# Optimization experiments

Measured on AMD Instinct MI355X. Metric: run time of the kernel, lower is better.

Reference implementation:

```python
import jax, jax.numpy as jnp
import numpy as np

A, B, S, E, H = 8, 64, 128, 512, 512


def _xavier(key, shape):
    fan_in, fan_out = shape[-2], shape[-1]
    limit = float(np.sqrt(6.0 / (fan_in + fan_out)))
    return jax.random.uniform(key, shape, jnp.float32, -limit, limit)


def setup_inputs() -> dict:
    key = jax.random.key(0)
    ks = jax.random.split(key, 8)
    inp = {
        "x": jax.random.normal(ks[0], (A, B, S, E), jnp.float32),
        "input2r": _xavier(ks[1], (A, E, H)),
        "input2z": _xavier(ks[2], (A, E, H)),
        "input2n": _xavier(ks[3], (A, E, H)),
        "hidden2r": _xavier(ks[4], (A, H, H)),
        "hidden2z": _xavier(ks[5], (A, H, H)),
        "hidden2n": _xavier(ks[6], (A, H, H)),
        "input2r_bias": jnp.zeros((A, H), jnp.float32),
        "input2z_bias": jnp.zeros((A, H), jnp.float32),
        "input2n_bias": jnp.zeros((A, H), jnp.float32),
        "hidden2r_bias": jnp.zeros((A, H), jnp.float32),
        "hidden2z_bias": jnp.zeros((A, H), jnp.float32),
        "hidden2n_bias": jnp.zeros((A, H), jnp.float32),
    }
    return inp


def _gru(x, input2r, input2z, input2n, input2r_bias, input2z_bias, input2n_bias,
         hidden2r, hidden2z, hidden2n, hidden2r_bias, hidden2z_bias, hidden2n_bias):
    # Precompute the input projections for all timesteps at once (same math,
    # hoisted out of the sequential loop): [A,B,S,H] -> scan over S.
    xr = jnp.einsum('abse,aeh->absh', x, input2r) + input2r_bias[:, None, None, :]
    xz = jnp.einsum('abse,aeh->absh', x, input2z) + input2z_bias[:, None, None, :]
    xn = jnp.einsum('abse,aeh->absh', x, input2n) + input2n_bias[:, None, None, :]
    # scan carries h: [A,B,H]; inputs have leading S axis.
    xr_t = jnp.moveaxis(xr, 2, 0)  # [S,A,B,H]
    xz_t = jnp.moveaxis(xz, 2, 0)
    xn_t = jnp.moveaxis(xn, 2, 0)

    hrb = hidden2r_bias[:, None, :]
    hzb = hidden2z_bias[:, None, :]
    hnb = hidden2n_bias[:, None, :]

    def step(h, inputs):
        xr_i, xz_i, xn_i = inputs
        r = jax.nn.sigmoid(xr_i + jnp.einsum('abh,ahk->abk', h, hidden2r) + hrb)
        z = jax.nn.sigmoid(xz_i + jnp.einsum('abh,ahk->abk', h, hidden2z) + hzb)
        n = jnp.tanh(xn_i + r * (jnp.einsum('abh,ahk->abk', h, hidden2n) + hnb))
        h_new = (1.0 - z) * n + z * h
        return h_new, h_new

    h0 = jnp.zeros((x.shape[0], x.shape[1], hidden2r.shape[-1]), x.dtype)
    h_last, outs = jax.lax.scan(step, h0, (xr_t, xz_t, xn_t))
    outputs = jnp.moveaxis(outs, 0, 2)  # [A,B,S,H]
    return outputs, h_last


def reference(x, input2r, input2z, input2n, input2r_bias, input2z_bias, input2n_bias,
              hidden2r, hidden2z, hidden2n, hidden2r_bias, hidden2z_bias, hidden2n_bias):
    return _gru(x, input2r, input2z, input2n, input2r_bias, input2z_bias, input2n_bias,
                hidden2r, hidden2z, hidden2n, hidden2r_bias, hidden2z_bias, hidden2n_bias)
```

## Files before the change

### kernel.cpp

```cpp
#include <hip/hip_runtime.h>

#define A_ 8
#define B_ 64
#define S_ 128
#define E_ 512
#define H_ 512

typedef float f32x4 __attribute__((ext_vector_type(4)));
typedef short s16x8 __attribute__((ext_vector_type(8)));

__device__ __forceinline__ float sigm(float v)   { return 1.f / (1.f + __expf(-v)); }
__device__ __forceinline__ float tanh_f(float v) { return 2.f / (1.f + __expf(-2.f * v)) - 1.f; }

__device__ __forceinline__ unsigned short f2bf(float f) {
  unsigned u = __builtin_bit_cast(unsigned, f);
  u += 0x7fffu + ((u >> 16) & 1u);
  return (unsigned short)(u >> 16);
}
__device__ __forceinline__ float bf2f(unsigned short b) {
  return __builtin_bit_cast(float, ((unsigned)b) << 16);
}

union U2 { unsigned long long u[2]; s16x8 v; };
union PK { uint4 u; unsigned short h[8]; };
union PH { s16x8 v; unsigned short h[8]; };

__global__ __launch_bounds__(256, 2) void gru_proj(
    const float* __restrict__ x,
    const float* __restrict__ wri, const float* __restrict__ wzi, const float* __restrict__ wni,
    const float* __restrict__ bri, const float* __restrict__ bzi, const float* __restrict__ bni,
    const float* __restrict__ brh, const float* __restrict__ bzh,
    unsigned short* __restrict__ xprz, float* __restrict__ xn_arr)
{
  const int b    = blockIdx.x;
  const int gate = blockIdx.y >> 2;
  const int n0   = (blockIdx.y & 3) * 128;
  const int a    = blockIdx.z;
  const int tid  = threadIdx.x;
  const int lane = tid & 63;
  const int wid  = tid >> 6;
  const int l15  = lane & 15;
  const int l4   = lane >> 4;

  const float* W  = gate == 0 ? wri : gate == 1 ? wzi : wni;
  const float* Wp = W + (size_t)a * E_ * H_;
  const float* xp = x + (size_t)(a * B_ + b) * S_ * E_;

  __shared__ short Af[4096];
  __shared__ short Bf[4096];

  f32x4 acc[2][8];
#pragma unroll
  for (int i = 0; i < 2; ++i)
#pragma unroll
    for (int j = 0; j < 8; ++j) acc[i][j] = (f32x4){0.f, 0.f, 0.f, 0.f};

  const int am  = tid >> 1;
  const int ah  = tid & 1;
  const int bnl = tid & 127;
  const int bo2 = (tid >> 7) * 2;

  for (int kt = 0; kt < E_; kt += 32) {
    const float* ap = xp + (size_t)am * E_ + kt + ah * 16;
    float4 a0 = *(const float4*)(ap);
    float4 a1 = *(const float4*)(ap + 4);
    float4 a2 = *(const float4*)(ap + 8);
    float4 a3 = *(const float4*)(ap + 12);
    PH pa0, pa1;
    pa0.h[0]=f2bf(a0.x); pa0.h[1]=f2bf(a0.y); pa0.h[2]=f2bf(a0.z); pa0.h[3]=f2bf(a0.w);
    pa0.h[4]=f2bf(a1.x); pa0.h[5]=f2bf(a1.y); pa0.h[6]=f2bf(a1.z); pa0.h[7]=f2bf(a1.w);
    pa1.h[0]=f2bf(a2.x); pa1.h[1]=f2bf(a2.y); pa1.h[2]=f2bf(a2.z); pa1.h[3]=f2bf(a2.w);
    pa1.h[4]=f2bf(a3.x); pa1.h[5]=f2bf(a3.y); pa1.h[6]=f2bf(a3.z); pa1.h[7]=f2bf(a3.w);
    int au = (am >> 4) * 64 + (ah * 2) * 16 + (am & 15);
    ((s16x8*)Af)[au]      = pa0.v;
    ((s16x8*)Af)[au + 16] = pa1.v;
#pragma unroll
    for (int oo = 0; oo < 2; ++oo) {
      int o = bo2 + oo;
      const float* wp2 = Wp + (size_t)(kt + o * 8) * H_ + n0 + bnl;
      PH pb;
#pragma unroll
      for (int j = 0; j < 8; ++j) pb.h[j] = f2bf(wp2[(size_t)j * H_]);
      ((s16x8*)Bf)[(bnl >> 4) * 64 + o * 16 + (bnl & 15)] = pb.v;
    }
    __syncthreads();
    s16x8 av0 = ((s16x8*)Af)[(wid * 2 + 0) * 64 + lane];
    s16x8 av1 = ((s16x8*)Af)[(wid * 2 + 1) * 64 + lane];
#pragma unroll
    for (int ns = 0; ns < 8; ++ns) {
      s16x8 bv = ((s16x8*)Bf)[ns * 64 + lane];
      acc[0][ns] = __builtin_amdgcn_mfma_f32_16x16x32_bf16(av0, bv, acc[0][ns], 0, 0, 0);
      acc[1][ns] = __builtin_amdgcn_mfma_f32_16x16x32_bf16(av1, bv, acc[1][ns], 0, 0, 0);
    }
    __syncthreads();
  }

#pragma unroll
  for (int ns = 0; ns < 8; ++ns) {
    int col = n0 + ns * 16 + l15;
    float bv;
    if (gate == 0)      bv = bri[a * H_ + col] + brh[a * H_ + col];
    else if (gate == 1) bv = bzi[a * H_ + col] + bzh[a * H_ + col];
    else                bv = bni[a * H_ + col];
#pragma unroll
    for (int ms = 0; ms < 2; ++ms) {
#pragma unroll
      for (int i = 0; i < 4; ++i) {
        int srow = wid * 32 + ms * 16 + l4 * 4 + i;
        size_t base = ((size_t)(a * S_ + srow) * B_ + b) * H_ + col;
        float v = acc[ms][ns][i] + bv;
        if (gate == 2) xn_arr[base] = v;
        else           xprz[base * 2 + gate] = f2bf(v);
      }
    }
  }
}

__global__ __launch_bounds__(256, 1) void gru_scan(
    const unsigned* __restrict__ xprz, const float* __restrict__ xn_arr,
    const float* __restrict__ wrh, const float* __restrict__ wzh, const float* __restrict__ wnh,
    const float* __restrict__ bnh,
    float* __restrict__ out, float* __restrict__ hlast,
    unsigned short* __restrict__ hbuf0, unsigned short* __restrict__ hbuf1,
    int* __restrict__ flags)
{
  __shared__ uint4 wflat[6144];

  const int wg    = blockIdx.x;
  const int G     = wg & 15;
  const int a     = G >> 1;
  const int hf    = G & 1;
  const int slice = wg >> 4;
  const int tid   = threadIdx.x;
  const int lane  = tid & 63;
  const int w     = tid >> 6;
  const int l15   = lane & 15;
  const int l4    = lane >> 4;
  const int mt    = w & 1;
  const int nt    = w >> 1;

  for (int idx = tid; idx < 6144; idx += 256) {
    int gate = idx >> 11;
    int rem  = idx & 2047;
    int kk   = rem >> 7;
    int rem2 = rem & 127;
    int nt_  = rem2 >> 6;
    int l    = rem2 & 63;
    int col   = slice * 32 + nt_ * 16 + (l & 15);
    int kbase = kk * 32 + (l >> 4) * 8;
    const float* W = gate == 0 ? wrh : gate == 1 ? wzh : wnh;
    const float* wp = W + ((size_t)(a * H_ + kbase)) * H_ + col;
    PK pk;
#pragma unroll
    for (int j = 0; j < 8; ++j) pk.h[j] = f2bf(wp[(size_t)j * H_]);
    wflat[idx] = pk.u;
  }
  __syncthreads();

  const int nc    = slice * 32 + nt * 16 + l15;
  const float vbnh = bnh[a * H_ + nc];
  const int halfb = (a * 2 + hf) * 16384;
  const int hbase = halfb + l4 * 256 + (mt * 16 + l15) * 8;
  int* flagsG = flags + G * (16 * 32);

  float hold[4] = {0.f, 0.f, 0.f, 0.f};
  float xr_[4], xz_[4], xn_[4];

#pragma unroll
  for (int i = 0; i < 4; ++i) {
    int b = hf * 32 + mt * 16 + l4 * 4 + i;
    size_t xo = ((size_t)(a * S_ + 0) * B_ + b) * H_ + nc;
    unsigned prz = xprz[xo];
    xr_[i] = bf2f((unsigned short)(prz & 0xffff));
    xz_[i] = bf2f((unsigned short)(prz >> 16));
    xn_[i] = xn_arr[xo];
  }

  const f32x4 zero4 = {0.f, 0.f, 0.f, 0.f};

  for (int s = 0; s < S_; ++s) {
    const unsigned short* hprev = (s & 1) ? hbuf0 : hbuf1;
    unsigned short*       hcur  = (s & 1) ? hbuf1 : hbuf0;

    U2 hh[16];
#pragma unroll
    for (int kk = 0; kk < 16; ++kk) {
      unsigned long long* p = (unsigned long long*)(hprev + hbase + kk * 1024);
      hh[kk].u[0] = __hip_atomic_load(p,     __ATOMIC_RELAXED, __HIP_MEMORY_SCOPE_AGENT);
      hh[kk].u[1] = __hip_atomic_load(p + 1, __ATOMIC_RELAXED, __HIP_MEMORY_SCOPE_AGENT);
    }
    f32x4 aR = zero4, aZ = zero4, aHN = zero4;
#pragma unroll
    for (int kk = 0; kk < 16; ++kk) {
      s16x8 bR = __builtin_bit_cast(s16x8, wflat[(kk)*128        + nt * 64 + lane]);
      s16x8 bZ = __builtin_bit_cast(s16x8, wflat[2048 + kk * 128 + nt * 64 + lane]);
      s16x8 bN = __builtin_bit_cast(s16x8, wflat[4096 + kk * 128 + nt * 64 + lane]);
      aR  = __builtin_amdgcn_mfma_f32_16x16x32_bf16(hh[kk].v, bR, aR, 0, 0, 0);
      aZ  = __builtin_amdgcn_mfma_f32_16x16x32_bf16(hh[kk].v, bZ, aZ, 0, 0, 0);
      aHN = __builtin_amdgcn_mfma_f32_16x16x32_bf16(hh[kk].v, bN, aHN, 0, 0, 0);
    }

    float hn4[4];
#pragma unroll
    for (int i = 0; i < 4; ++i) {
      float rg = sigm(xr_[i] + aR[i]);
      float zg = sigm(xz_[i] + aZ[i]);
      float ng = tanh_f(xn_[i] + rg * (aHN[i] + vbnh));
      hn4[i] = (1.f - zg) * ng + zg * hold[i];
      hold[i] = hn4[i];
    }

#pragma unroll
    for (int i = 0; i < 4; ++i) {
      int r = mt * 16 + l4 * 4 + i;
      unsigned short nb = f2bf(hn4[i]);
      unsigned other = __shfl_xor((unsigned)nb, 1);
      if ((lane & 1) == 0) {
        unsigned val = (unsigned)nb | (other << 16);
        __hip_atomic_store((unsigned*)(hcur + halfb + (nc >> 3) * 256 + r * 8 + (nc & 6)),
                           val, __ATOMIC_RELAXED, __HIP_MEMORY_SCOPE_AGENT);
      }
    }
    __syncthreads();
    asm volatile("" ::: "memory");
    if (tid == 0)
      __hip_atomic_store(flagsG + slice * 32, s + 1,
                         __ATOMIC_RELAXED, __HIP_MEMORY_SCOPE_AGENT);

#pragma unroll
    for (int i = 0; i < 4; ++i) {
      int b = hf * 32 + mt * 16 + l4 * 4 + i;
      out[((size_t)(a * B_ + b) * S_ + s) * H_ + nc] = hn4[i];
    }
    if (s == S_ - 1) {
#pragma unroll
      for (int i = 0; i < 4; ++i) {
        int b = hf * 32 + mt * 16 + l4 * 4 + i;
        hlast[(size_t)(a * B_ + b) * H_ + nc] = hn4[i];
      }
    } else {
#pragma unroll
      for (int i = 0; i < 4; ++i) {
        int b = hf * 32 + mt * 16 + l4 * 4 + i;
        size_t xo = ((size_t)(a * S_ + (s + 1)) * B_ + b) * H_ + nc;
        unsigned prz = xprz[xo];
        xr_[i] = bf2f((unsigned short)(prz & 0xffff));
        xz_[i] = bf2f((unsigned short)(prz >> 16));
        xn_[i] = xn_arr[xo];
      }
      const int target = s + 1;
      for (;;) {
        int v = __hip_atomic_load(flagsG + (lane & 15) * 32,
                                  __ATOMIC_RELAXED, __HIP_MEMORY_SCOPE_AGENT);
        if (__all(v >= target)) break;
      }
      asm volatile("" ::: "memory");
    }
  }
}

__global__ __launch_bounds__(256, 1) void gru_persist(
    const float* __restrict__ x,
    const float* __restrict__ wri, const float* __restrict__ wzi, const float* __restrict__ wni,
    const float* __restrict__ wrh, const float* __restrict__ wzh, const float* __restrict__ wnh,
    const float* __restrict__ bri, const float* __restrict__ bzi, const float* __restrict__ bni,
    const float* __restrict__ brh, const float* __restrict__ bzh, const float* __restrict__ bnh,
    float* __restrict__ out, float* __restrict__ hlast,
    unsigned short* __restrict__ hbuf0, unsigned short* __restrict__ hbuf1,
    int* __restrict__ flags)
{
  __shared__ uint4 wflat[6144];
  const int wg = blockIdx.x, a = wg >> 5, slice = wg & 31, n0 = slice << 4;
  const int tid = threadIdx.x, lane = tid & 63, wid = tid >> 6;
  const int l15 = lane & 15, l4 = lane >> 4, b0w = wid << 4;

  for (int idx = tid; idx < 6144; idx += 256) {
    int set = idx / 3072, rem = idx - set * 3072, gate = rem >> 10;
    int rem2 = rem & 1023, kk = rem2 >> 6, l = rem2 & 63;
    int c = l & 15, kbase = kk * 32 + (l >> 4) * 8;
    const float* W = (set == 0) ? (gate == 0 ? wri : gate == 1 ? wzi : wni)
                                : (gate == 0 ? wrh : gate == 1 ? wzh : wnh);
    const float* wp = W + ((size_t)(a * 512 + kbase)) * 512 + n0 + c;
    PK pk;
#pragma unroll
    for (int j = 0; j < 8; ++j) pk.h[j] = f2bf(wp[(size_t)j * 512]);
    wflat[idx] = pk.u;
  }
  __syncthreads();

  const int nc = n0 + l15;
  const float vbri = bri[a*512+nc], vbzi = bzi[a*512+nc], vbni = bni[a*512+nc];
  const float vbrh = brh[a*512+nc], vbzh = bzh[a*512+nc], vbnh = bnh[a*512+nc];
  const float* xrow = x + (size_t)(a * 64 + b0w + l15) * 65536 + l4 * 8;
  const int hbase = ((a * 64 + l4) * 64 + b0w + l15) * 8;
  int* flagsA = flags + a * 64;
  const f32x4 zero4 = {0.f, 0.f, 0.f, 0.f};
  f32x4 aR, aZ, aXN, aHN;

  auto xpart = [&](int sv) {
    const float* xp = xrow + (size_t)sv * 512;
    aR = zero4; aZ = zero4; aXN = zero4;
#pragma unroll
    for (int kk = 0; kk < 16; ++kk) {
      float4 x0 = *reinterpret_cast<const float4*>(xp + kk * 32);
      float4 x1 = *reinterpret_cast<const float4*>(xp + kk * 32 + 4);
      PH af;
      af.h[0]=f2bf(x0.x); af.h[1]=f2bf(x0.y); af.h[2]=f2bf(x0.z); af.h[3]=f2bf(x0.w);
      af.h[4]=f2bf(x1.x); af.h[5]=f2bf(x1.y); af.h[6]=f2bf(x1.z); af.h[7]=f2bf(x1.w);
      s16x8 bR = __builtin_bit_cast(s16x8, wflat[(kk)*64+lane]);
      s16x8 bZ = __builtin_bit_cast(s16x8, wflat[(16+kk)*64+lane]);
      s16x8 bN = __builtin_bit_cast(s16x8, wflat[(32+kk)*64+lane]);
      aR  = __builtin_amdgcn_mfma_f32_16x16x32_bf16(af.v, bR, aR, 0,0,0);
      aZ  = __builtin_amdgcn_mfma_f32_16x16x32_bf16(af.v, bZ, aZ, 0,0,0);
      aXN = __builtin_amdgcn_mfma_f32_16x16x32_bf16(af.v, bN, aXN, 0,0,0);
    }
  };

  xpart(0);
  for (int s = 0; s < S_; ++s) {
    const unsigned short* hprev = (s & 1) ? hbuf0 : hbuf1;
    unsigned short*       hcur  = (s & 1) ? hbuf1 : hbuf0;
    aHN = zero4;
#pragma unroll
    for (int kk = 0; kk < 16; ++kk) {
      unsigned long long* p = (unsigned long long*)(hprev + hbase + kk * 2048);
      U2 uu;
      uu.u[0] = __hip_atomic_load(p,   __ATOMIC_RELAXED, __HIP_MEMORY_SCOPE_AGENT);
      uu.u[1] = __hip_atomic_load(p+1, __ATOMIC_RELAXED, __HIP_MEMORY_SCOPE_AGENT);
      s16x8 bR = __builtin_bit_cast(s16x8, wflat[(48+kk)*64+lane]);
      s16x8 bZ = __builtin_bit_cast(s16x8, wflat[(64+kk)*64+lane]);
      s16x8 bN = __builtin_bit_cast(s16x8, wflat[(80+kk)*64+lane]);
      aR  = __builtin_amdgcn_mfma_f32_16x16x32_bf16(uu.v, bR, aR, 0,0,0);
      aZ  = __builtin_amdgcn_mfma_f32_16x16x32_bf16(uu.v, bZ, aZ, 0,0,0);
      aHN = __builtin_amdgcn_mfma_f32_16x16x32_bf16(uu.v, bN, aHN, 0,0,0);
    }
#pragma unroll
    for (int i = 0; i < 4; ++i) {
      int r = b0w + l4 * 4 + i;
      unsigned* hop = (unsigned*)(hprev + ((a*64 + (nc>>3))*64 + r)*8 + (nc&6));
      unsigned pair = __hip_atomic_load(hop, __ATOMIC_RELAXED, __HIP_MEMORY_SCOPE_AGENT);
      float hold = bf2f((nc & 1) ? (unsigned short)(pair >> 16) : (unsigned short)(pair & 0xffff));
      float rg = sigm(aR[i] + vbri + vbrh);
      float zg = sigm(aZ[i] + vbzi + vbzh);
      float ng = tanh_f(aXN[i] + vbni + rg * (aHN[i] + vbnh));
      float hnew = (1.f - zg) * ng + zg * hold;
      out[((size_t)(a*64 + r)*128 + s)*512 + nc] = hnew;
      if (s == S_ - 1) hlast[(size_t)(a*64 + r)*512 + nc] = hnew;
      unsigned short nb = f2bf(hnew);
      unsigned other = __shfl_xor((unsigned)nb, 1);
      if ((lane & 1) == 0) {
        unsigned val = (unsigned)nb | (other << 16);
        __hip_atomic_store((unsigned*)(hcur + ((a*64 + (nc>>3))*64 + r)*8 + (nc&6)),
                           val, __ATOMIC_RELAXED, __HIP_MEMORY_SCOPE_AGENT);
      }
    }
    __syncthreads();
    if (tid == 0)
      __hip_atomic_store(flagsA + slice, s + 1, __ATOMIC_RELEASE, __HIP_MEMORY_SCOPE_AGENT);
    if (s < S_ - 1) {
      xpart(s + 1);
      const int target = s + 1;
      for (;;) {
        int v = __hip_atomic_load(flagsA + (lane & 31), __ATOMIC_ACQUIRE, __HIP_MEMORY_SCOPE_AGENT);
        if (__all(v >= target)) break;
        __builtin_amdgcn_s_sleep(1);
      }
    }
  }
}

extern "C" void kernel_launch(void* const* d_in, const int* in_sizes, int n_in,
                              void* d_out, int out_size, void* d_ws, size_t ws_size,
                              hipStream_t stream)
{
  const float* x   = (const float*)d_in[0];
  const float* wri = (const float*)d_in[1];
  const float* wzi = (const float*)d_in[2];
  const float* wni = (const float*)d_in[3];
  const float* wrh = (const float*)d_in[4];
  const float* wzh = (const float*)d_in[5];
  const float* wnh = (const float*)d_in[6];
  const float* bri = (const float*)d_in[7];
  const float* bzi = (const float*)d_in[8];
  const float* bni = (const float*)d_in[9];
  const float* brh = (const float*)d_in[10];
  const float* bzh = (const float*)d_in[11];
  const float* bnh = (const float*)d_in[12];

  float* out   = (float*)d_out;
  float* hlast = out + (size_t)A_ * B_ * S_ * H_;

  const size_t XPRZ  = (size_t)A_ * S_ * B_ * H_;
  const size_t HBUF  = (size_t)A_ * 64 * 64 * 8;
  const size_t FLAGS_B = (size_t)16 * 16 * 32 * sizeof(int);
  const size_t need_new = XPRZ * 4 * 2 + HBUF * 2 * 2 + FLAGS_B;
  const size_t need_old = HBUF * 2 * 2 + 2048;

  if (ws_size >= need_new) {
    unsigned* xprz = (unsigned*)d_ws;
    float* xn_arr  = (float*)((char*)d_ws + XPRZ * 4);
    unsigned short* hbuf0 = (unsigned short*)((char*)d_ws + XPRZ * 8);
    unsigned short* hbuf1 = hbuf0 + HBUF;
    int* flags = (int*)(hbuf1 + HBUF);
    hipMemsetAsync(hbuf0, 0, HBUF * 2 * 2 + FLAGS_B, stream);
    gru_proj<<<dim3(64, 12, 8), 256, 0, stream>>>(x, wri, wzi, wni,
                                                  bri, bzi, bni, brh, bzh,
                                                  (unsigned short*)xprz, xn_arr);
    gru_scan<<<256, 256, 0, stream>>>(xprz, xn_arr, wrh, wzh, wnh, bnh,
                                      out, hlast, hbuf0, hbuf1, flags);
  } else if (ws_size >= need_old) {
    unsigned short* hbuf0 = (unsigned short*)d_ws;
    unsigned short* hbuf1 = hbuf0 + HBUF;
    int* flags = (int*)(hbuf1 + HBUF);
    hipMemsetAsync(d_ws, 0, need_old, stream);
    gru_persist<<<256, 256, 0, stream>>>(x, wri, wzi, wni, wrh, wzh, wnh,
                                         bri, bzi, bni, brh, bzh, bnh,
                                         out, hlast, hbuf0, hbuf1, flags);
  }
}
```

Before: 775.2 us.

## Replace flag barrier with poison-value data-driven sync on quad-buffered hidden state

```diff
diff --git a/kernel.cpp b/kernel.cpp
--- a/kernel.cpp
+++ b/kernel.cpp
@@ -5,6 +5,7 @@
 #define S_ 128
 #define E_ 512
 #define H_ 512
+#define HBUF1 262144
 
 typedef float f32x4 __attribute__((ext_vector_type(4)));
 typedef short s16x8 __attribute__((ext_vector_type(8)));
@@ -121,8 +122,7 @@
     const float* __restrict__ wrh, const float* __restrict__ wzh, const float* __restrict__ wnh,
     const float* __restrict__ bnh,
     float* __restrict__ out, float* __restrict__ hlast,
-    unsigned short* __restrict__ hbuf0, unsigned short* __restrict__ hbuf1,
-    int* __restrict__ flags)
+    unsigned short* __restrict__ hbufs)
 {
   __shared__ uint4 wflat[6144];
 
@@ -161,7 +161,7 @@
   const float vbnh = bnh[a * H_ + nc];
   const int halfb = (a * 2 + hf) * 16384;
   const int hbase = halfb + l4 * 256 + (mt * 16 + l15) * 8;
-  int* flagsG = flags + G * (16 * 32);
+  const int hsto  = halfb + (nc >> 3) * 256 + (nc & 6);
 
   float hold[4] = {0.f, 0.f, 0.f, 0.f};
   float xr_[4], xz_[4], xn_[4];
@@ -179,20 +179,35 @@
   const f32x4 zero4 = {0.f, 0.f, 0.f, 0.f};
 
   for (int s = 0; s < S_; ++s) {
-    const unsigned short* hprev = (s & 1) ? hbuf0 : hbuf1;
-    unsigned short*       hcur  = (s & 1) ? hbuf1 : hbuf0;
+    const unsigned short* hprev = hbufs + (size_t)((s + 3) & 3) * HBUF1;
+    unsigned short*       hcur  = hbufs + (size_t)(s & 3)       * HBUF1;
+    unsigned short*       hpoi  = hbufs + (size_t)((s + 2) & 3) * HBUF1;
 
     U2 hh[16];
+    if (s == 0) {
+#pragma unroll
+      for (int kk = 0; kk < 16; ++kk) { hh[kk].u[0] = 0ull; hh[kk].u[1] = 0ull; }
+    } else {
+      for (;;) {
+        bool ok = true;
+#pragma unroll
+        for (int kk = 0; kk < 16; ++kk) {
+          const unsigned long long* p =
+              (const unsigned long long*)(hprev + hbase + kk * 1024);
+          unsigned long long v0 = __hip_atomic_load(p,     __ATOMIC_RELAXED, __HIP_MEMORY_SCOPE_AGENT);
+          unsigned long long v1 = __hip_atomic_load(p + 1, __ATOMIC_RELAXED, __HIP_MEMORY_SCOPE_AGENT);
+          hh[kk].u[0] = v0; hh[kk].u[1] = v1;
+          ok = ok & ((unsigned)v0 != 0xFFFFFFFFu) & ((unsigned)(v0 >> 32) != 0xFFFFFFFFu)
+                  & ((unsigned)v1 != 0xFFFFFFFFu) & ((unsigned)(v1 >> 32) != 0xFFFFFFFFu);
+        }
+        if (__all(ok)) break;
+      }
+    }
+
+    f32x4 aR = zero4, aZ = zero4, aHN = zero4;
 #pragma unroll
     for (int kk = 0; kk < 16; ++kk) {
-      unsigned long long* p = (unsigned long long*)(hprev + hbase + kk * 1024);
-      hh[kk].u[0] = __hip_atomic_load(p,     __ATOMIC_RELAXED, __HIP_MEMORY_SCOPE_AGENT);
-      hh[kk].u[1] = __hip_atomic_load(p + 1, __ATOMIC_RELAXED, __HIP_MEMORY_SCOPE_AGENT);
-    }
-    f32x4 aR = zero4, aZ = zero4, aHN = zero4;
-#pragma unroll
-    for (int kk = 0; kk < 16; ++kk) {
-      s16x8 bR = __builtin_bit_cast(s16x8, wflat[(kk)*128        + nt * 64 + lane]);
+      s16x8 bR = __builtin_bit_cast(s16x8, wflat[kk * 128        + nt * 64 + lane]);
       s16x8 bZ = __builtin_bit_cast(s16x8, wflat[2048 + kk * 128 + nt * 64 + lane]);
       s16x8 bN = __builtin_bit_cast(s16x8, wflat[4096 + kk * 128 + nt * 64 + lane]);
       aR  = __builtin_amdgcn_mfma_f32_16x16x32_bf16(hh[kk].v, bR, aR, 0, 0, 0);
@@ -217,15 +232,17 @@
       unsigned other = __shfl_xor((unsigned)nb, 1);
       if ((lane & 1) == 0) {
         unsigned val = (unsigned)nb | (other << 16);
-        __hip_atomic_store((unsigned*)(hcur + halfb + (nc >> 3) * 256 + r * 8 + (nc & 6)),
-                           val, __ATOMIC_RELAXED, __HIP_MEMORY_SCOPE_AGENT);
-      }
-    }
-    __syncthreads();
-    asm volatile("" ::: "memory");
-    if (tid == 0)
-      __hip_atomic_store(flagsG + slice * 32, s + 1,
-                         __ATOMIC_RELAXED, __HIP_MEMORY_SCOPE_AGENT);
+        __hip_atomic_store((unsigned*)(hcur + hsto + r * 8), val,
+                           __ATOMIC_RELAXED, __HIP_MEMORY_SCOPE_AGENT);
+      }
+    }
+#pragma unroll
+    for (int i = 0; i < 4; ++i) {
+      int r = mt * 16 + l4 * 4 + i;
+      if ((lane & 1) == 0)
+        __hip_atomic_store((unsigned*)(hpoi + hsto + r * 8), 0xFFFFFFFFu,
+                           __ATOMIC_RELAXED, __HIP_MEMORY_SCOPE_AGENT);
+    }
 
 #pragma unroll
     for (int i = 0; i < 4; ++i) {
@@ -248,14 +265,8 @@
         xz_[i] = bf2f((unsigned short)(prz >> 16));
         xn_[i] = xn_arr[xo];
       }
-      const int target = s + 1;
-      for (;;) {
-        int v = __hip_atomic_load(flagsG + (lane & 15) * 32,
-                                  __ATOMIC_RELAXED, __HIP_MEMORY_SCOPE_AGENT);
-        if (__all(v >= target)) break;
-      }
-      asm volatile("" ::: "memory");
-    }
+    }
+    asm volatile("s_waitcnt vmcnt(0)" ::: "memory");
   }
 }
 
@@ -391,27 +402,23 @@
   float* hlast = out + (size_t)A_ * B_ * S_ * H_;
 
   const size_t XPRZ  = (size_t)A_ * S_ * B_ * H_;
-  const size_t HBUF  = (size_t)A_ * 64 * 64 * 8;
-  const size_t FLAGS_B = (size_t)16 * 16 * 32 * sizeof(int);
-  const size_t need_new = XPRZ * 4 * 2 + HBUF * 2 * 2 + FLAGS_B;
-  const size_t need_old = HBUF * 2 * 2 + 2048;
+  const size_t need_new = XPRZ * 8 + (size_t)4 * HBUF1 * 2;
+  const size_t need_old = (size_t)HBUF1 * 4 + 2048;
 
   if (ws_size >= need_new) {
     unsigned* xprz = (unsigned*)d_ws;
     float* xn_arr  = (float*)((char*)d_ws + XPRZ * 4);
-    unsigned short* hbuf0 = (unsigned short*)((char*)d_ws + XPRZ * 8);
-    unsigned short* hbuf1 = hbuf0 + HBUF;
-    int* flags = (int*)(hbuf1 + HBUF);
-    hipMemsetAsync(hbuf0, 0, HBUF * 2 * 2 + FLAGS_B, stream);
+    unsigned short* hbufs = (unsigned short*)((char*)d_ws + XPRZ * 8);
+    hipMemsetAsync(hbufs, 0xFF, (size_t)4 * HBUF1 * 2, stream);
     gru_proj<<<dim3(64, 12, 8), 256, 0, stream>>>(x, wri, wzi, wni,
                                                   bri, bzi, bni, brh, bzh,
                                                   (unsigned short*)xprz, xn_arr);
     gru_scan<<<256, 256, 0, stream>>>(xprz, xn_arr, wrh, wzh, wnh, bnh,
-                                      out, hlast, hbuf0, hbuf1, flags);
+                                      out, hlast, hbufs);
   } else if (ws_size >= need_old) {
     unsigned short* hbuf0 = (unsigned short*)d_ws;
-    unsigned short* hbuf1 = hbuf0 + HBUF;
-    int* flags = (int*)(hbuf1 + HBUF);
+    unsigned short* hbuf1 = hbuf0 + HBUF1;
+    int* flags = (int*)(hbuf1 + HBUF1);
     hipMemsetAsync(d_ws, 0, need_old, stream);
     gru_persist<<<256, 256, 0, stream>>>(x, wri, wzi, wni, wrh, wzh, wnh,
                                          bri, bzi, bni, brh, bzh, bnh,
```

New measurement: 1.042 ms. 1.34x slower.

## Fuse three gate projections per block and pack r/z as one 32-bit store

Applied to the files above, without the earlier changes.

```diff
diff --git a/kernel.cpp b/kernel.cpp
--- a/kernel.cpp
+++ b/kernel.cpp
@@ -30,11 +30,10 @@
     const float* __restrict__ wri, const float* __restrict__ wzi, const float* __restrict__ wni,
     const float* __restrict__ bri, const float* __restrict__ bzi, const float* __restrict__ bni,
     const float* __restrict__ brh, const float* __restrict__ bzh,
-    unsigned short* __restrict__ xprz, float* __restrict__ xn_arr)
+    unsigned* __restrict__ xprz, float* __restrict__ xn_arr)
 {
   const int b    = blockIdx.x;
-  const int gate = blockIdx.y >> 2;
-  const int n0   = (blockIdx.y & 3) * 128;
+  const int n0   = blockIdx.y * 64;
   const int a    = blockIdx.z;
   const int tid  = threadIdx.x;
   const int lane = tid & 63;
@@ -42,23 +41,21 @@
   const int l15  = lane & 15;
   const int l4   = lane >> 4;
 
-  const float* W  = gate == 0 ? wri : gate == 1 ? wzi : wni;
-  const float* Wp = W + (size_t)a * E_ * H_;
   const float* xp = x + (size_t)(a * B_ + b) * S_ * E_;
 
   __shared__ short Af[4096];
-  __shared__ short Bf[4096];
-
-  f32x4 acc[2][8];
-#pragma unroll
-  for (int i = 0; i < 2; ++i)
-#pragma unroll
-    for (int j = 0; j < 8; ++j) acc[i][j] = (f32x4){0.f, 0.f, 0.f, 0.f};
-
-  const int am  = tid >> 1;
-  const int ah  = tid & 1;
-  const int bnl = tid & 127;
-  const int bo2 = (tid >> 7) * 2;
+  __shared__ short Bf[6144];
+
+  f32x4 acc[3][2][4];
+#pragma unroll
+  for (int g = 0; g < 3; ++g)
+#pragma unroll
+    for (int m = 0; m < 2; ++m)
+#pragma unroll
+      for (int c = 0; c < 4; ++c) acc[g][m][c] = (f32x4){0.f, 0.f, 0.f, 0.f};
+
+  const int am = tid >> 1;
+  const int ah = tid & 1;
 
   for (int kt = 0; kt < E_; kt += 32) {
     const float* ap = xp + (size_t)am * E_ + kt + ah * 16;
@@ -74,43 +71,54 @@
     int au = (am >> 4) * 64 + (ah * 2) * 16 + (am & 15);
     ((s16x8*)Af)[au]      = pa0.v;
     ((s16x8*)Af)[au + 16] = pa1.v;
-#pragma unroll
-    for (int oo = 0; oo < 2; ++oo) {
-      int o = bo2 + oo;
-      const float* wp2 = Wp + (size_t)(kt + o * 8) * H_ + n0 + bnl;
+
+#pragma unroll
+    for (int ii = 0; ii < 3; ++ii) {
+      int idx  = tid + ii * 256;
+      int gate = idx >> 8;
+      int rem  = idx & 255;
+      int l    = rem & 63;
+      int col  = n0 + ((rem >> 6) << 4) + (l & 15);
+      int kb   = kt + (l >> 4) * 8;
+      const float* W = gate == 0 ? wri : gate == 1 ? wzi : wni;
+      const float* wp2 = W + (size_t)(a * E_ + kb) * H_ + col;
       PH pb;
 #pragma unroll
       for (int j = 0; j < 8; ++j) pb.h[j] = f2bf(wp2[(size_t)j * H_]);
-      ((s16x8*)Bf)[(bnl >> 4) * 64 + o * 16 + (bnl & 15)] = pb.v;
+      ((s16x8*)Bf)[idx] = pb.v;
     }
     __syncthreads();
+
     s16x8 av0 = ((s16x8*)Af)[(wid * 2 + 0) * 64 + lane];
     s16x8 av1 = ((s16x8*)Af)[(wid * 2 + 1) * 64 + lane];
 #pragma unroll
-    for (int ns = 0; ns < 8; ++ns) {
-      s16x8 bv = ((s16x8*)Bf)[ns * 64 + lane];
-      acc[0][ns] = __builtin_amdgcn_mfma_f32_16x16x32_bf16(av0, bv, acc[0][ns], 0, 0, 0);
-      acc[1][ns] = __builtin_amdgcn_mfma_f32_16x16x32_bf16(av1, bv, acc[1][ns], 0, 0, 0);
-    }
+    for (int g = 0; g < 3; ++g)
+#pragma unroll
+      for (int cs = 0; cs < 4; ++cs) {
+        s16x8 bv = ((s16x8*)Bf)[g * 256 + cs * 64 + lane];
+        acc[g][0][cs] = __builtin_amdgcn_mfma_f32_16x16x32_bf16(av0, bv, acc[g][0][cs], 0, 0, 0);
+        acc[g][1][cs] = __builtin_amdgcn_mfma_f32_16x16x32_bf16(av1, bv, acc[g][1][cs], 0, 0, 0);
+      }
     __syncthreads();
   }
 
 #pragma unroll
-  for (int ns = 0; ns < 8; ++ns) {
-    int col = n0 + ns * 16 + l15;
-    float bv;
-    if (gate == 0)      bv = bri[a * H_ + col] + brh[a * H_ + col];
-    else if (gate == 1) bv = bzi[a * H_ + col] + bzh[a * H_ + col];
-    else                bv = bni[a * H_ + col];
-#pragma unroll
-    for (int ms = 0; ms < 2; ++ms) {
+  for (int cs = 0; cs < 4; ++cs) {
+    int col = n0 + cs * 16 + l15;
+    float br = bri[a * H_ + col] + brh[a * H_ + col];
+    float bz = bzi[a * H_ + col] + bzh[a * H_ + col];
+    float bn = bni[a * H_ + col];
+#pragma unroll
+    for (int m = 0; m < 2; ++m) {
 #pragma unroll
       for (int i = 0; i < 4; ++i) {
-        int srow = wid * 32 + ms * 16 + l4 * 4 + i;
+        int srow = wid * 32 + m * 16 + l4 * 4 + i;
         size_t base = ((size_t)(a * S_ + srow) * B_ + b) * H_ + col;
-        float v = acc[ms][ns][i] + bv;
-        if (gate == 2) xn_arr[base] = v;
-        else           xprz[base * 2 + gate] = f2bf(v);
+        float rv = acc[0][m][cs][i] + br;
+        float zv = acc[1][m][cs][i] + bz;
+        float nv = acc[2][m][cs][i] + bn;
+        xprz[base]   = (unsigned)f2bf(rv) | ((unsigned)f2bf(zv) << 16);
+        xn_arr[base] = nv;
       }
     }
   }
@@ -192,7 +200,7 @@
     f32x4 aR = zero4, aZ = zero4, aHN = zero4;
 #pragma unroll
     for (int kk = 0; kk < 16; ++kk) {
-      s16x8 bR = __builtin_bit_cast(s16x8, wflat[(kk)*128        + nt * 64 + lane]);
+      s16x8 bR = __builtin_bit_cast(s16x8, wflat[kk * 128        + nt * 64 + lane]);
       s16x8 bZ = __builtin_bit_cast(s16x8, wflat[2048 + kk * 128 + nt * 64 + lane]);
       s16x8 bN = __builtin_bit_cast(s16x8, wflat[4096 + kk * 128 + nt * 64 + lane]);
       aR  = __builtin_amdgcn_mfma_f32_16x16x32_bf16(hh[kk].v, bR, aR, 0, 0, 0);
@@ -403,9 +411,9 @@
     unsigned short* hbuf1 = hbuf0 + HBUF;
     int* flags = (int*)(hbuf1 + HBUF);
     hipMemsetAsync(hbuf0, 0, HBUF * 2 * 2 + FLAGS_B, stream);
-    gru_proj<<<dim3(64, 12, 8), 256, 0, stream>>>(x, wri, wzi, wni,
-                                                  bri, bzi, bni, brh, bzh,
-                                                  (unsigned short*)xprz, xn_arr);
+    gru_proj<<<dim3(64, 8, 8), 256, 0, stream>>>(x, wri, wzi, wni,
+                                                 bri, bzi, bni, brh, bzh,
+                                                 xprz, xn_arr);
     gru_scan<<<256, 256, 0, stream>>>(xprz, xn_arr, wrh, wzh, wnh, bnh,
                                       out, hlast, hbuf0, hbuf1, flags);
   } else if (ws_size >= need_old) {
```

After: 756.0 us (median of 2 runs). 2.5% less time.
